# Optimization experiments

Hardware: AMD Instinct MI355X
Metric: run time of the kernel (lower is better)

## Reference

```python
import jax, jax.numpy as jnp
import numpy as np

BINS = 10


def setup_inputs() -> dict:
    key = jax.random.key(0)
    k1, k2 = jax.random.split(key)
    x = jax.random.uniform(k1, (16384, 2048), dtype=jnp.float32, minval=1e-4, maxval=1.0 - 1e-4)
    target = jax.random.uniform(k2, (16384, 2048), dtype=jnp.float32)
    return {"x": x, "target": target}


def reference(x, target):
    # gradient magnitude (detached in original)
    g = jnp.abs(jax.lax.stop_gradient(x) - target)
    # _g2bin: floor(g * (bins - 0.0001)) -> integer bin ids in [0, BINS-1]
    bin_idx = jnp.floor(g * (BINS - 1e-4)).astype(jnp.int32)
    # histogram (replaces the serialized per-bin python loop)
    bin_count = jnp.bincount(bin_idx.ravel(), length=BINS).astype(jnp.float32)
    N = x.shape[0] * x.shape[1]
    nonempty_bins = jnp.sum(bin_count > 0).astype(jnp.float32)
    gd = jnp.clip(bin_count * nonempty_bins, 1.0, None)
    beta = N / gd  # [BINS]
    # BCE on probabilities, reweighted by gathered beta
    loss = -(target * jnp.log(x) + (1.0 - target) * jnp.log(1.0 - x))
    loss = loss * beta[bin_idx]
    return jnp.mean(loss)
```

## Files before the change

kernel.cpp:

```cpp
#include <hip/hip_runtime.h>

#define BINS 10
#define NTHR 9

template<bool GUARD>
__device__ __forceinline__ void accum_elem(float xx, float tt, bool live,
                                           float* __restrict__ S,
                                           unsigned* __restrict__ wcnt,
                                           float& s_total)
{
    float y = fabsf(xx - tt) * 9.9999f;
    float l1 = __log2f(xx);
    float l2 = __log2f(1.0f - xx);
    float s = __builtin_fmaf(tt, l1 - l2, l2);
    if (GUARD) {
        y = live ? y : -1.0f;
        s = live ? s : 0.0f;
    }
    s_total += s;
#pragma unroll
    for (int j = 0; j < NTHR; ++j) {
        bool p = (y >= (float)(j + 1));
        S[j] += p ? s : 0.0f;
        wcnt[j] += (unsigned)__popcll(__ballot(p));
    }
}

template<bool GUARD>
__device__ __forceinline__ void accum4(float4 xv, float4 tv, bool live,
                                       float* __restrict__ S,
                                       unsigned* __restrict__ wcnt, float& st)
{
    accum_elem<GUARD>(xv.x, tv.x, live, S, wcnt, st);
    accum_elem<GUARD>(xv.y, tv.y, live, S, wcnt, st);
    accum_elem<GUARD>(xv.z, tv.z, live, S, wcnt, st);
    accum_elem<GUARD>(xv.w, tv.w, live, S, wcnt, st);
}

__global__ __launch_bounds__(256, 4) void ghm_partial(
    const float* __restrict__ x, const float* __restrict__ t,
    float* __restrict__ psum, unsigned* __restrict__ pcnt,
    int n4, long long n_total, int nblocks)
{
    float S[NTHR];
    unsigned wcnt[NTHR];
    float s_total = 0.0f;
#pragma unroll
    for (int j = 0; j < NTHR; ++j) { S[j] = 0.0f; wcnt[j] = 0u; }

    const float4* __restrict__ x4 = (const float4*)x;
    const float4* __restrict__ t4 = (const float4*)t;
    const int tid = blockIdx.x * blockDim.x + threadIdx.x;
    const int stride = gridDim.x * blockDim.x;
    const int iters = n4 / (2 * stride);

    if (iters > 0) {
        long long i = tid;
        float4 ax = x4[i],          at_ = t4[i];
        float4 bx = x4[i + stride], bt  = t4[i + stride];
        for (int k = 0; ; ++k) {
            bool more = (k + 1 < iters);
            long long nx = i + 2LL * stride;
            float4 cx, ct, dx, dt;
            if (more) {
                cx = x4[nx];          ct = t4[nx];
                dx = x4[nx + stride]; dt = t4[nx + stride];
            }
            accum4<false>(ax, at_, true, S, wcnt, s_total);
            accum4<false>(bx, bt,  true, S, wcnt, s_total);
            if (!more) break;
            ax = cx; at_ = ct; bx = dx; bt = dt; i = nx;
        }
    }

    long long r0 = (long long)tid + (long long)iters * 2LL * stride;
    long long blk_min = (long long)blockIdx.x * blockDim.x + (long long)iters * 2LL * stride;
    if (blk_min < n4) {
#pragma unroll
        for (int q = 0; q < 2; ++q) {
            long long r = r0 + (long long)q * stride;
            bool live = r < n4;
            int ri = live ? (int)r : 0;
            float4 xv = x4[ri], tv = t4[ri];
            accum4<true>(xv, tv, live, S, wcnt, s_total);
        }
    }

    long long tail_base = (long long)n4 * 4;
    if (blockIdx.x == 0 && tail_base < n_total) {
        long long e = tail_base + threadIdx.x;
        bool live = e < n_total;
        long long ei = live ? e : (n_total - 1);
        accum_elem<true>(x[ei], t[ei], live, S, wcnt, s_total);
    }

#pragma unroll
    for (int off = 32; off > 0; off >>= 1) s_total += __shfl_down(s_total, off, 64);
#pragma unroll
    for (int j = 0; j < NTHR; ++j) {
#pragma unroll
        for (int off = 32; off > 0; off >>= 1) S[j] += __shfl_down(S[j], off, 64);
    }

    __shared__ float s_sum[4][NTHR + 1];
    __shared__ unsigned s_cnt[4][NTHR];
    int lane = threadIdx.x & 63;
    int wv = threadIdx.x >> 6;
    if (lane == 0) {
        s_sum[wv][0] = s_total;
#pragma unroll
        for (int j = 0; j < NTHR; ++j) { s_sum[wv][j + 1] = S[j]; s_cnt[wv][j] = wcnt[j]; }
    }
    __syncthreads();
    if (threadIdx.x < NTHR + 1) {
        int r = threadIdx.x;
        float s = 0.0f;
#pragma unroll
        for (int w = 0; w < 4; ++w) s += s_sum[w][r];
        psum[(size_t)r * nblocks + blockIdx.x] = s;
        if (r < NTHR) {
            unsigned c = 0u;
#pragma unroll
            for (int w = 0; w < 4; ++w) c += s_cnt[w][r];
            pcnt[(size_t)r * nblocks + blockIdx.x] = c;
        }
    }
}

__global__ __launch_bounds__(256) void ghm_final(
    const float* __restrict__ psum, const unsigned* __restrict__ pcnt,
    float* __restrict__ out, int nblocks, float Nf, long long N)
{
    float rs[NTHR + 1];
    unsigned rc[NTHR];
#pragma unroll
    for (int r = 0; r < NTHR + 1; ++r) rs[r] = 0.0f;
#pragma unroll
    for (int r = 0; r < NTHR; ++r) rc[r] = 0u;

    for (int i = threadIdx.x; i < nblocks; i += 256) {
#pragma unroll
        for (int r = 0; r < NTHR + 1; ++r) rs[r] += psum[(size_t)r * nblocks + i];
#pragma unroll
        for (int r = 0; r < NTHR; ++r) rc[r] += pcnt[(size_t)r * nblocks + i];
    }

#pragma unroll
    for (int r = 0; r < NTHR + 1; ++r) {
#pragma unroll
        for (int off = 32; off > 0; off >>= 1) rs[r] += __shfl_down(rs[r], off, 64);
    }
#pragma unroll
    for (int r = 0; r < NTHR; ++r) {
#pragma unroll
        for (int off = 32; off > 0; off >>= 1) rc[r] += (unsigned)__shfl_down((int)rc[r], off, 64);
    }

    __shared__ float s_sum[4][NTHR + 1];
    __shared__ unsigned s_cnt[4][NTHR];
    int lane = threadIdx.x & 63;
    int wv = threadIdx.x >> 6;
    if (lane == 0) {
#pragma unroll
        for (int r = 0; r < NTHR + 1; ++r) s_sum[wv][r] = rs[r];
#pragma unroll
        for (int r = 0; r < NTHR; ++r) s_cnt[wv][r] = rc[r];
    }
    __syncthreads();

    if (threadIdx.x == 0) {
        float Sc[BINS + 1];
        float Cc[BINS + 1];
#pragma unroll
        for (int r = 0; r < NTHR + 1; ++r) {
            float s = 0.0f;
#pragma unroll
            for (int w = 0; w < 4; ++w) s += s_sum[w][r];
            Sc[r] = s;
        }
        Sc[BINS] = 0.0f;
        Cc[0] = (float)N;
#pragma unroll
        for (int r = 0; r < NTHR; ++r) {
            unsigned c = 0u;
#pragma unroll
            for (int w = 0; w < 4; ++w) c += s_cnt[w][r];
            Cc[r + 1] = (float)c;
        }
        Cc[BINS] = 0.0f;

        float nonempty = 0.0f;
        float cnt[BINS], sb[BINS];
#pragma unroll
        for (int b = 0; b < BINS; ++b) {
            cnt[b] = Cc[b] - Cc[b + 1];
            sb[b] = Sc[b] - Sc[b + 1];
            nonempty += (cnt[b] > 0.0f) ? 1.0f : 0.0f;
        }
        float total = 0.0f;
#pragma unroll
        for (int b = 0; b < BINS; ++b) {
            float gd = cnt[b] * nonempty;
            gd = gd < 1.0f ? 1.0f : gd;
            total += sb[b] * (Nf / gd);
        }
        const float LN2 = 0.69314718055994530942f;
        out[0] = -LN2 * total / Nf;
    }
}

extern "C" void kernel_launch(void* const* d_in, const int* in_sizes, int n_in,
                              void* d_out, int out_size, void* d_ws, size_t ws_size,
                              hipStream_t stream) {
    const float* x = (const float*)d_in[0];
    const float* t = (const float*)d_in[1];
    float* out = (float*)d_out;

    long long N = (long long)in_sizes[0];
    int n4 = (int)(N / 4);

    int nblocks = 2048;
    size_t per_block = (size_t)(NTHR + 1) * sizeof(float) + (size_t)NTHR * sizeof(unsigned);
    size_t maxb = ws_size / per_block;
    if ((size_t)nblocks > maxb) nblocks = (int)maxb;
    if (nblocks < 1) nblocks = 1;

    float* psum = (float*)d_ws;
    unsigned* pcnt = (unsigned*)(psum + (size_t)(NTHR + 1) * nblocks);

    ghm_partial<<<nblocks, 256, 0, stream>>>(x, t, psum, pcnt, n4, N, nblocks);
    ghm_final<<<1, 256, 0, stream>>>(psum, pcnt, out, nblocks, (float)N, N);
}
```

Measured before the change: 289.4 us.

## Stage input tiles through LDS with async global-to-LDS double buffering

```diff
diff --git a/kernel.cpp b/kernel.cpp
--- a/kernel.cpp
+++ b/kernel.cpp
@@ -2,6 +2,16 @@
 
 #define BINS 10
 #define NTHR 9
+#define TPB 256
+#define F4PT 2
+#define TILE_F4 (TPB * F4PT)
+
+__device__ __forceinline__ void stage16(const float4* g, float4* l) {
+    __builtin_amdgcn_global_load_lds(
+        (const __attribute__((address_space(1))) unsigned int*)g,
+        (__attribute__((address_space(3))) unsigned int*)l,
+        16, 0, 0);
+}
 
 template<bool GUARD>
 __device__ __forceinline__ void accum_elem(float xx, float tt, bool live,
@@ -37,11 +47,14 @@
     accum_elem<GUARD>(xv.w, tv.w, live, S, wcnt, st);
 }
 
-__global__ __launch_bounds__(256, 4) void ghm_partial(
+__global__ __launch_bounds__(TPB) void ghm_partial(
     const float* __restrict__ x, const float* __restrict__ t,
     float* __restrict__ psum, unsigned* __restrict__ pcnt,
     int n4, long long n_total, int nblocks)
 {
+    __shared__ float4 sx[2][TILE_F4];
+    __shared__ float4 st_[2][TILE_F4];
+
     float S[NTHR];
     unsigned wcnt[NTHR];
     float s_total = 0.0f;
@@ -50,37 +63,54 @@
 
     const float4* __restrict__ x4 = (const float4*)x;
     const float4* __restrict__ t4 = (const float4*)t;
-    const int tid = blockIdx.x * blockDim.x + threadIdx.x;
-    const int stride = gridDim.x * blockDim.x;
-    const int iters = n4 / (2 * stride);
+    const int tid = threadIdx.x;
+    const int wv = tid >> 6;
+    const int wbase = wv * 64;
+    const long long iter_stride = (long long)nblocks * TILE_F4;
+    const int iters = (int)((long long)n4 / iter_stride);
 
     if (iters > 0) {
-        long long i = tid;
-        float4 ax = x4[i],          at_ = t4[i];
-        float4 bx = x4[i + stride], bt  = t4[i + stride];
+        {
+            long long gb = (long long)blockIdx.x * TILE_F4;
+#pragma unroll
+            for (int j = 0; j < F4PT; ++j) {
+                stage16(&x4[gb + j * TPB + tid], &sx[0][j * TPB + wbase]);
+                stage16(&t4[gb + j * TPB + tid], &st_[0][j * TPB + wbase]);
+            }
+        }
+        __syncthreads();
+
         for (int k = 0; ; ++k) {
-            bool more = (k + 1 < iters);
-            long long nx = i + 2LL * stride;
-            float4 cx, ct, dx, dt;
-            if (more) {
-                cx = x4[nx];          ct = t4[nx];
-                dx = x4[nx + stride]; dt = t4[nx + stride];
+            int cur = k & 1;
+            if (k + 1 < iters) {
+                long long gb = (long long)(k + 1) * iter_stride + (long long)blockIdx.x * TILE_F4;
+                int nxt = cur ^ 1;
+#pragma unroll
+                for (int j = 0; j < F4PT; ++j) {
+                    stage16(&x4[gb + j * TPB + tid], &sx[nxt][j * TPB + wbase]);
+                    stage16(&t4[gb + j * TPB + tid], &st_[nxt][j * TPB + wbase]);
+                }
             }
-            accum4<false>(ax, at_, true, S, wcnt, s_total);
-            accum4<false>(bx, bt,  true, S, wcnt, s_total);
-            if (!more) break;
-            ax = cx; at_ = ct; bx = dx; bt = dt; i = nx;
-        }
-    }
-
-    long long r0 = (long long)tid + (long long)iters * 2LL * stride;
-    long long blk_min = (long long)blockIdx.x * blockDim.x + (long long)iters * 2LL * stride;
-    if (blk_min < n4) {
-#pragma unroll
-        for (int q = 0; q < 2; ++q) {
-            long long r = r0 + (long long)q * stride;
+#pragma unroll
+            for (int j = 0; j < F4PT; ++j) {
+                float4 xv = sx[cur][j * TPB + tid];
+                float4 tv = st_[cur][j * TPB + tid];
+                accum4<false>(xv, tv, true, S, wcnt, s_total);
+            }
+            if (k + 1 >= iters) break;
+            __syncthreads();
+        }
+    }
+
+    long long done = (long long)iters * iter_stride;
+    if (done < n4) {
+        long long gtid = (long long)blockIdx.x * TPB + tid;
+        long long total_thr = (long long)nblocks * TPB;
+#pragma unroll
+        for (int q = 0; q < F4PT; ++q) {
+            long long r = done + gtid + (long long)q * total_thr;
             bool live = r < n4;
-            int ri = live ? (int)r : 0;
+            long long ri = live ? r : 0;
             float4 xv = x4[ri], tv = t4[ri];
             accum4<true>(xv, tv, live, S, wcnt, s_total);
         }
@@ -88,7 +118,7 @@
 
     long long tail_base = (long long)n4 * 4;
     if (blockIdx.x == 0 && tail_base < n_total) {
-        long long e = tail_base + threadIdx.x;
+        long long e = tail_base + tid;
         bool live = e < n_total;
         long long ei = live ? e : (n_total - 1);
         accum_elem<true>(x[ei], t[ei], live, S, wcnt, s_total);
@@ -102,26 +132,26 @@
         for (int off = 32; off > 0; off >>= 1) S[j] += __shfl_down(S[j], off, 64);
     }
 
-    __shared__ float s_sum[4][NTHR + 1];
-    __shared__ unsigned s_cnt[4][NTHR];
-    int lane = threadIdx.x & 63;
-    int wv = threadIdx.x >> 6;
+    __shared__ float red_s[4][NTHR + 1];
+    __shared__ unsigned red_c[4][NTHR];
+    int lane = tid & 63;
+    __syncthreads();
     if (lane == 0) {
-        s_sum[wv][0] = s_total;
-#pragma unroll
-        for (int j = 0; j < NTHR; ++j) { s_sum[wv][j + 1] = S[j]; s_cnt[wv][j] = wcnt[j]; }
+        red_s[wv][0] = s_total;
+#pragma unroll
+        for (int j = 0; j < NTHR; ++j) { red_s[wv][j + 1] = S[j]; red_c[wv][j] = wcnt[j]; }
     }
     __syncthreads();
-    if (threadIdx.x < NTHR + 1) {
-        int r = threadIdx.x;
+    if (tid < NTHR + 1) {
+        int r = tid;
         float s = 0.0f;
 #pragma unroll
-        for (int w = 0; w < 4; ++w) s += s_sum[w][r];
+        for (int w = 0; w < 4; ++w) s += red_s[w][r];
         psum[(size_t)r * nblocks + blockIdx.x] = s;
         if (r < NTHR) {
             unsigned c = 0u;
 #pragma unroll
-            for (int w = 0; w < 4; ++w) c += s_cnt[w][r];
+            for (int w = 0; w < 4; ++w) c += red_c[w][r];
             pcnt[(size_t)r * nblocks + blockIdx.x] = c;
         }
     }
@@ -228,6 +258,6 @@
     float* psum = (float*)d_ws;
     unsigned* pcnt = (unsigned*)(psum + (size_t)(NTHR + 1) * nblocks);
 
-    ghm_partial<<<nblocks, 256, 0, stream>>>(x, t, psum, pcnt, n4, N, nblocks);
+    ghm_partial<<<nblocks, TPB, 0, stream>>>(x, t, psum, pcnt, n4, N, nblocks);
     ghm_final<<<1, 256, 0, stream>>>(psum, pcnt, out, nblocks, (float)N, N);
 }
```

Measured after the change: 285.6 us. About the same (-1.3%).
